# Optimization experiments

Hardware: AMD Instinct MI355X
Metric: run time of the kernel (lower is better)

Reference implementation:

```python
import jax, jax.numpy as jnp
import numpy as np

N, E, F_IN = 100000, 600000, 128
HID, NCLS = 128, 2
# ratio=0.8 applied three times: ceil(0.8*100000), ceil(0.8*80000), ceil(0.8*64000)
K1, K2, K3 = 80000, 64000, 51200


def setup_inputs() -> dict:
    key = jax.random.key(0)
    k = jax.random.split(key, 16)
    s = 0.05
    p = {}
    p['x'] = jax.random.normal(k[0], (N, F_IN), dtype=jnp.float32)
    p['edge_index'] = jax.random.randint(k[1], (2, E), 0, N)
    # GraphConv i: out = lin_rel(sum_j x_j) + lin_root(x_i); lin_root has no bias (PyG)
    p['Wr1'] = jax.random.normal(k[2], (HID, F_IN), jnp.float32) * s
    p['br1'] = jnp.zeros((HID,), jnp.float32)
    p['Wroot1'] = jax.random.normal(k[3], (HID, F_IN), jnp.float32) * s
    p['pw1'] = jax.random.normal(k[4], (HID,), jnp.float32) * s
    p['Wr2'] = jax.random.normal(k[5], (HID, HID), jnp.float32) * s
    p['br2'] = jnp.zeros((HID,), jnp.float32)
    p['Wroot2'] = jax.random.normal(k[6], (HID, HID), jnp.float32) * s
    p['pw2'] = jax.random.normal(k[7], (HID,), jnp.float32) * s
    p['Wr3'] = jax.random.normal(k[8], (HID, HID), jnp.float32) * s
    p['br3'] = jnp.zeros((HID,), jnp.float32)
    p['Wroot3'] = jax.random.normal(k[9], (HID, HID), jnp.float32) * s
    p['pw3'] = jax.random.normal(k[10], (HID,), jnp.float32) * s
    p['W_lin1'] = jax.random.normal(k[11], (HID, 2 * HID), jnp.float32) * s
    p['b_lin1'] = jnp.zeros((HID,), jnp.float32)
    p['W_lin2'] = jax.random.normal(k[12], (64, HID), jnp.float32) * s
    p['b_lin2'] = jnp.zeros((64,), jnp.float32)
    p['W_lin3'] = jax.random.normal(k[13], (NCLS, 64), jnp.float32) * s
    p['b_lin3'] = jnp.zeros((NCLS,), jnp.float32)
    return p


def _gconv(x, src, dst, emask, Wr, br, Wroot):
    # PyG GraphConv(aggr='add'): masked edges contribute zero (== removed edge)
    msg = x[src] * emask[:, None].astype(x.dtype)           # [E, F]
    agg = jax.ops.segment_sum(msg, dst, num_segments=x.shape[0])
    return agg @ Wr.T + br + x @ Wroot.T


def _topk_pool(x, src, dst, emask, w, k):
    # PyG TopKPooling: score = tanh((x.w)/||w||); keep top-k nodes; x = x[perm]*score[perm]
    score = jnp.tanh((x @ w) / jnp.linalg.norm(w))
    vals, perm = jax.lax.top_k(score, k)
    x_new = x[perm] * vals[:, None]
    new_idx = jnp.full((x.shape[0],), -1, jnp.int32).at[perm].set(
        jnp.arange(k, dtype=jnp.int32))
    ns, nd = new_idx[src], new_idx[dst]
    valid = emask & (ns >= 0) & (nd >= 0)
    return x_new, jnp.where(valid, ns, 0), jnp.where(valid, nd, 0), valid


def _readout(x):
    # single graph (batch=None): gmp || gap -> [1, 2F]
    return jnp.concatenate([x.max(axis=0), x.mean(axis=0)])[None, :]


def reference(x, edge_index, Wr1, br1, Wroot1, pw1, Wr2, br2, Wroot2, pw2,
              Wr3, br3, Wroot3, pw3, W_lin1, b_lin1, W_lin2, b_lin2, W_lin3, b_lin3):
    src = edge_index[0].astype(jnp.int32)
    dst = edge_index[1].astype(jnp.int32)
    emask = jnp.ones((src.shape[0],), dtype=bool)

    h = jax.nn.relu(_gconv(x, src, dst, emask, Wr1, br1, Wroot1))
    h, src, dst, emask = _topk_pool(h, src, dst, emask, pw1, K1)
    r1 = _readout(h)

    h = jax.nn.relu(_gconv(h, src, dst, emask, Wr2, br2, Wroot2))
    h, src, dst, emask = _topk_pool(h, src, dst, emask, pw2, K2)
    r2 = _readout(h)

    h = jax.nn.relu(_gconv(h, src, dst, emask, Wr3, br3, Wroot3))
    h, src, dst, emask = _topk_pool(h, src, dst, emask, pw3, K3)
    r3 = _readout(h)

    z = r1 + r2 + r3                                        # [1, 256]
    z = jax.nn.relu(z @ W_lin1.T + b_lin1)                  # dropout: inference no-op
    z = jax.nn.relu(z @ W_lin2.T + b_lin2)
    return z @ W_lin3.T + b_lin3                            # [1, num_classes]
```

## Files before the change

### kernel.cpp

```cpp
#include <hip/hip_runtime.h>
#include <hip/hip_bf16.h>
#include <math.h>

#define N0 100000
#define E0 600000
#define KP1 80000
#define KP2 64000
#define KP3 51200
#define F 128
#define SCAN_CHUNK 1024
#define NCHUNK ((N0 + SCAN_CHUNK - 1) / SCAN_CHUNK)
#define MAXGB 6400

typedef __attribute__((ext_vector_type(8))) short short8;
typedef __attribute__((ext_vector_type(8))) unsigned short ushort8;
typedef __attribute__((ext_vector_type(4))) float f32x4;

__device__ __forceinline__ unsigned fkey(float f) {
    unsigned u = __float_as_uint(f);
    return u ^ ((u & 0x80000000u) ? 0xFFFFFFFFu : 0x80000000u);
}
__device__ __forceinline__ unsigned short f2b(float f) {
    __hip_bfloat16 h = __float2bfloat16(f);
    return *(unsigned short*)&h;
}
__device__ __forceinline__ float b2f(unsigned short u) {
    __hip_bfloat16 h;
    *(unsigned short*)&h = u;
    return __bfloat162float(h);
}

__global__ __launch_bounds__(256) void cvt4K(const float* __restrict__ in,
                                             unsigned short* __restrict__ out, int n4,
                                             unsigned* __restrict__ bar, unsigned* __restrict__ hist,
                                             unsigned* __restrict__ cnt, int* __restrict__ orig) {
    int i = blockIdx.x * 256 + threadIdx.x;
    if (blockIdx.x == 0) {
        if (threadIdx.x < 16) bar[threadIdx.x] = 0u;
        hist[threadIdx.x] = 0u;
    }
    if (i < N0) { cnt[i] = 0u; orig[i] = i; }
    if (i >= n4) return;
    float4 v = *(const float4*)(in + (size_t)i * 4);
    *(ushort4*)(out + (size_t)i * 4) = make_ushort4(f2b(v.x), f2b(v.y), f2b(v.z), f2b(v.w));
}

__global__ __launch_bounds__(256) void cvtWAllK(const float* __restrict__ a0, const float* __restrict__ a1,
                                                const float* __restrict__ a2, const float* __restrict__ a3,
                                                const float* __restrict__ a4, const float* __restrict__ a5,
                                                unsigned short* __restrict__ o) {
    int m = blockIdx.y;
    const float* src = (m == 0) ? a0 : (m == 1) ? a1 : (m == 2) ? a2 : (m == 3) ? a3 : (m == 4) ? a4 : a5;
    int i = blockIdx.x * 256 + threadIdx.x;
    float4 v = *(const float4*)(src + (size_t)i * 4);
    *(ushort4*)(o + (size_t)m * 16384 + (size_t)i * 4) = make_ushort4(f2b(v.x), f2b(v.y), f2b(v.z), f2b(v.w));
}

__global__ __launch_bounds__(128) void pwnK(const float* __restrict__ p0, const float* __restrict__ p1,
                                            const float* __restrict__ p2, float* __restrict__ pwn) {
    __shared__ float sh[128];
    int l = blockIdx.x, t = threadIdx.x;
    const float* p = (l == 0) ? p0 : (l == 1) ? p1 : p2;
    float v = p[t];
    sh[t] = v * v;
    __syncthreads();
    for (int off = 64; off; off >>= 1) {
        if (t < off) sh[t] += sh[t + off];
        __syncthreads();
    }
    pwn[l * 128 + t] = v / sqrtf(sh[0]);
}

__global__ __launch_bounds__(256) void histDstK(const int* __restrict__ dst, unsigned* __restrict__ cnt) {
    int e = blockIdx.x * 256 + threadIdx.x;
    if (e < E0) atomicAdd(&cnt[dst[e]], 1u);
}

__global__ __launch_bounds__(256) void scanReduceK(const unsigned* __restrict__ cnt,
                                                   unsigned* __restrict__ chunkSum, int nbins) {
    __shared__ unsigned sh[256];
    int base = blockIdx.x * SCAN_CHUNK + threadIdx.x * 4;
    unsigned s = 0;
#pragma unroll
    for (int i = 0; i < 4; i++) { int b = base + i; if (b < nbins) s += cnt[b]; }
    sh[threadIdx.x] = s;
    __syncthreads();
    for (int off = 128; off; off >>= 1) {
        if (threadIdx.x < off) sh[threadIdx.x] += sh[threadIdx.x + off];
        __syncthreads();
    }
    if (threadIdx.x == 0) chunkSum[blockIdx.x] = sh[0];
}

__global__ void scanChunksK(const unsigned* __restrict__ chunkSum, unsigned* __restrict__ chunkOff,
                            int nchunks, unsigned* __restrict__ totalOut) {
    if (threadIdx.x == 0) {
        unsigned run = 0;
        for (int i = 0; i < nchunks; i++) { chunkOff[i] = run; run += chunkSum[i]; }
        *totalOut = run;
    }
}

__global__ __launch_bounds__(256) void scanFinalK(const unsigned* __restrict__ cntIn,
                                                  unsigned* __restrict__ cnt,
                                                  const unsigned* __restrict__ chunkOff,
                                                  unsigned* __restrict__ rowptr, int nbins) {
    __shared__ unsigned sh[256];
    int t = threadIdx.x;
    int base = blockIdx.x * SCAN_CHUNK + t * 4;
    unsigned c[4], s = 0;
#pragma unroll
    for (int i = 0; i < 4; i++) { int b = base + i; c[i] = (b < nbins) ? cntIn[b] : 0u; s += c[i]; }
    sh[t] = s;
    __syncthreads();
    for (int off = 1; off < 256; off <<= 1) {
        unsigned v = (t >= off) ? sh[t - off] : 0u;
        __syncthreads();
        sh[t] += v;
        __syncthreads();
    }
    unsigned basep = chunkOff[blockIdx.x] + sh[t] - s;
#pragma unroll
    for (int i = 0; i < 4; i++) {
        int b = base + i;
        if (b < nbins) { rowptr[b] = basep; basep += c[i]; cnt[b] = 0u; }
    }
}

__global__ __launch_bounds__(256) void scatterFillK(const int* __restrict__ src,
                                                    const int* __restrict__ dst,
                                                    const unsigned* __restrict__ rowptr,
                                                    unsigned* __restrict__ fill,
                                                    int* __restrict__ sortedSrc) {
    int e = blockIdx.x * 256 + threadIdx.x;
    if (e >= E0) return;
    int d = dst[e];
    unsigned p = rowptr[d] + atomicAdd(&fill[d], 1u);
    sortedSrc[p] = src[e];
}

__global__ __launch_bounds__(256) void aggSegB(const unsigned short* __restrict__ x,
                                               const int* __restrict__ srcCur,
                                               const unsigned* __restrict__ rowptr,
                                               const int* __restrict__ orig,
                                               unsigned short* __restrict__ agg, int n) {
    int g = blockIdx.x * 16 + (threadIdx.x >> 4);
    int q = threadIdx.x & 15;
    if (g >= n) return;
    int d = orig[g];
    unsigned e0 = rowptr[d], e1 = rowptr[d + 1];
    float a[8];
#pragma unroll
    for (int j = 0; j < 8; j++) a[j] = 0.f;
    unsigned e = e0;
    for (; e + 4 <= e1; e += 4) {
        int s0 = srcCur[e], s1 = srcCur[e + 1], s2 = srcCur[e + 2], s3 = srcCur[e + 3];
        ushort8 v0 = *(const ushort8*)(x + (size_t)(s0 < 0 ? 0 : s0) * F + q * 8);
        ushort8 v1 = *(const ushort8*)(x + (size_t)(s1 < 0 ? 0 : s1) * F + q * 8);
        ushort8 v2 = *(const ushort8*)(x + (size_t)(s2 < 0 ? 0 : s2) * F + q * 8);
        ushort8 v3 = *(const ushort8*)(x + (size_t)(s3 < 0 ? 0 : s3) * F + q * 8);
        float m0 = s0 < 0 ? 0.f : 1.f, m1 = s1 < 0 ? 0.f : 1.f;
        float m2 = s2 < 0 ? 0.f : 1.f, m3 = s3 < 0 ? 0.f : 1.f;
#pragma unroll
        for (int j = 0; j < 8; j++) {
            a[j] = fmaf(b2f(v0[j]), m0, a[j]);
            a[j] = fmaf(b2f(v1[j]), m1, a[j]);
            a[j] = fmaf(b2f(v2[j]), m2, a[j]);
            a[j] = fmaf(b2f(v3[j]), m3, a[j]);
        }
    }
    for (; e < e1; e++) {
        int s = srcCur[e];
        if (s < 0) continue;
        ushort8 v = *(const ushort8*)(x + (size_t)s * F + q * 8);
#pragma unroll
        for (int j = 0; j < 8; j++) a[j] += b2f(v[j]);
    }
    ushort8 o;
#pragma unroll
    for (int j = 0; j < 8; j++) o[j] = f2b(a[j]);
    *(ushort8*)(agg + (size_t)g * F + q * 8) = o;
}

#define CPAD 40
__global__ __launch_bounds__(256) void convM(const unsigned short* __restrict__ A0,
                                             const unsigned short* __restrict__ A1,
                                             const unsigned short* __restrict__ W0,
                                             const unsigned short* __restrict__ W1,
                                             const float* __restrict__ br,
                                             const float* __restrict__ pwn,
                                             unsigned short* __restrict__ hbf,
                                             float* __restrict__ sc,
                                             unsigned* __restrict__ keys,
                                             unsigned* __restrict__ hist,
                                             unsigned* __restrict__ st,
                                             unsigned* __restrict__ done,
                                             int n, int k, int nbGrid) {
    __shared__ unsigned short As[128 * CPAD];
    __shared__ unsigned short Bs[128 * CPAD];
    __shared__ unsigned selh[256];
    int tid = threadIdx.x;
    int w = tid >> 6, l = tid & 63;
    int r = l & 15, g = l >> 4;
    int bm = blockIdx.x * 128;
    int srow = tid >> 2, q4 = tid & 3;

    selh[tid] = 0u;

    f32x4 acc[2][8];
#pragma unroll
    for (int m = 0; m < 2; m++)
#pragma unroll
        for (int c = 0; c < 8; c++) acc[m][c] = (f32x4){0.f, 0.f, 0.f, 0.f};

    for (int ph = 0; ph < 2; ph++) {
        const unsigned short* A = ph ? A1 : A0;
        const unsigned short* W = ph ? W1 : W0;
        for (int kk = 0; kk < 128; kk += 32) {
            __syncthreads();
#pragma unroll
            for (int h2 = 0; h2 < 2; h2++) {
                int rr = srow + h2 * 64;
                uint4 av = make_uint4(0u, 0u, 0u, 0u);
                if (bm + rr < n) av = *(const uint4*)(A + (size_t)(bm + rr) * F + kk + q4 * 8);
                *(uint4*)(&As[rr * CPAD + q4 * 8]) = av;
                uint4 wv = *(const uint4*)(W + (size_t)rr * F + kk + q4 * 8);
                *(uint4*)(&Bs[rr * CPAD + q4 * 8]) = wv;
            }
            __syncthreads();
            short8 af[2], bf[8];
#pragma unroll
            for (int m = 0; m < 2; m++)
                af[m] = *(const short8*)(&As[(w * 32 + m * 16 + r) * CPAD + g * 8]);
#pragma unroll
            for (int c = 0; c < 8; c++)
                bf[c] = *(const short8*)(&Bs[(c * 16 + r) * CPAD + g * 8]);
#pragma unroll
            for (int m = 0; m < 2; m++)
#pragma unroll
                for (int c = 0; c < 8; c++)
                    acc[m][c] = __builtin_amdgcn_mfma_f32_16x16x32_bf16(af[m], bf[c], acc[m][c], 0, 0, 0);
        }
    }

    float pd[2][4];
#pragma unroll
    for (int m = 0; m < 2; m++)
#pragma unroll
        for (int j = 0; j < 4; j++) pd[m][j] = 0.f;

#pragma unroll
    for (int c = 0; c < 8; c++) {
        int col = c * 16 + r;
        float bias = br[col];
        float pwc = pwn[col];
#pragma unroll
        for (int m = 0; m < 2; m++) {
#pragma unroll
            for (int j = 0; j < 4; j++) {
                int row = bm + w * 32 + m * 16 + g * 4 + j;
                float h = fmaxf(acc[m][c][j] + bias, 0.f);
                pd[m][j] += h * pwc;
                if (row < n) hbf[(size_t)row * F + col] = f2b(h);
            }
        }
    }
#pragma unroll
    for (int m = 0; m < 2; m++) {
#pragma unroll
        for (int j = 0; j < 4; j++) {
            float p = pd[m][j];
            p += __shfl_xor(p, 1);
            p += __shfl_xor(p, 2);
            p += __shfl_xor(p, 4);
            p += __shfl_xor(p, 8);
            if (r == 0) {
                int row = bm + w * 32 + m * 16 + g * 4 + j;
                if (row < n) {
                    float s = tanhf(p);
                    sc[row] = s;
                    unsigned key = fkey(s);
                    keys[row] = key;
                    atomicAdd(&selh[key >> 24], 1u);
                }
            }
        }
    }

    __syncthreads();
    if (selh[tid]) atomicAdd(&hist[tid], selh[tid]);
    __syncthreads();
    __shared__ bool lastS;
    if (tid == 0) {
        __threadfence();
        lastS = (atomicAdd(done, 1u) == (unsigned)(nbGrid - 1));
    }
    __syncthreads();
    if (!lastS) return;
    selh[tid] = atomicExch(&hist[tid], 0u);
    __syncthreads();
    if (tid == 0) {
        unsigned krem = (unsigned)k, cum = 0, pfx = 0;
        for (int bch = 255; bch >= 0; bch--) {
            unsigned cc = selh[bch];
            if (cum + cc >= krem) {
                pfx = ((unsigned)bch) << 24;
                krem -= cum;
                break;
            }
            cum += cc;
        }
        atomicExch(&st[0], pfx);
        atomicExch(&st[1], krem);
        *done = 0u;
    }
}

__global__ __launch_bounds__(256) void histSelK(const unsigned* __restrict__ keys, int n,
                                                int p, unsigned* __restrict__ st,
                                                unsigned* __restrict__ hist,
                                                unsigned* __restrict__ done, int nb) {
    __shared__ unsigned lh[256];
    __shared__ bool last;
    int tid = threadIdx.x;
    lh[tid] = 0;
    __syncthreads();
    unsigned prefix = st[0];
    int i = blockIdx.x * 256 + tid;
    if (i < n) {
        unsigned key = keys[i];
        bool m = ((key >> (32 - 8 * p)) == (prefix >> (32 - 8 * p)));
        if (m) atomicAdd(&lh[(key >> (24 - 8 * p)) & 255u], 1u);
    }
    __syncthreads();
    if (lh[tid]) atomicAdd(&hist[tid], lh[tid]);
    __syncthreads();
    if (tid == 0) {
        __threadfence();
        last = (atomicAdd(done, 1u) == (unsigned)(nb - 1));
    }
    __syncthreads();
    if (!last) return;
    lh[tid] = atomicExch(&hist[tid], 0u);
    __syncthreads();
    if (tid == 0) {
        unsigned krem = st[1], cum = 0;
        for (int b = 255; b >= 0; b--) {
            unsigned c = lh[b];
            if (cum + c >= krem) {
                st[0] |= ((unsigned)b) << (24 - 8 * p);
                st[1] = krem - cum;
                break;
            }
            cum += c;
        }
        *done = 0u;
    }
}

__global__ __launch_bounds__(256) void countsK(const unsigned* __restrict__ keys, int n,
                                               const unsigned* __restrict__ st,
                                               unsigned* __restrict__ bGT, unsigned* __restrict__ bEQ,
                                               unsigned* __restrict__ sGT, unsigned* __restrict__ sEQ,
                                               unsigned* __restrict__ done, int nb) {
    __shared__ int cg_, ce_;
    __shared__ bool last;
    __shared__ unsigned sgl[128], seq[128];
    int tid = threadIdx.x;
    if (tid == 0) { cg_ = 0; ce_ = 0; }
    __syncthreads();
    unsigned t = st[0];
    int g = 0, e = 0;
    for (int it = 0; it < 4; it++) {
        int i = blockIdx.x * 1024 + it * 256 + tid;
        if (i < n) {
            unsigned k = keys[i];
            g += (k > t);
            e += (k == t);
        }
    }
    atomicAdd(&cg_, g);
    atomicAdd(&ce_, e);
    __syncthreads();
    if (tid == 0) {
        bGT[blockIdx.x] = (unsigned)cg_;
        bEQ[blockIdx.x] = (unsigned)ce_;
        __threadfence();
        last = (atomicAdd(done, 1u) == (unsigned)(nb - 1));
    }
    __syncthreads();
    if (!last) return;
    if (tid < nb && tid < 128) { sgl[tid] = atomicAdd(&bGT[tid], 0u); seq[tid] = atomicAdd(&bEQ[tid], 0u); }
    __syncthreads();
    if (tid == 0) {
        unsigned gs = 0, es = 0;
        for (int b = 0; b < nb; b++) {
            atomicExch(&sGT[b], gs);
            atomicExch(&sEQ[b], es);
            gs += sgl[b];
            es += seq[b];
        }
        *done = 0u;
    }
}

__global__ __launch_bounds__(256) void markOrigK(const unsigned* __restrict__ keys, int n,
                                                 const unsigned* __restrict__ st,
                                                 const unsigned* __restrict__ sGT,
                                                 const unsigned* __restrict__ sEQ,
                                                 int* __restrict__ nidx,
                                                 const int* __restrict__ origIn,
                                                 int* __restrict__ origOut, int doNext) {
    __shared__ int wG[4], wE[4];
    __shared__ int runG, runE;
    int tid = threadIdx.x, wv = tid >> 6, lane = tid & 63;
    if (tid == 0) { runG = 0; runE = 0; }
    unsigned t = st[0];
    int needEq = (int)st[1];
    int gOff = (int)atomicAdd((unsigned*)&sGT[blockIdx.x], 0u);
    int eOff = (int)atomicAdd((unsigned*)&sEQ[blockIdx.x], 0u);
    unsigned long long mlt = (((unsigned long long)1) << lane) - 1ull;
    __syncthreads();
    for (int it = 0; it < 4; it++) {
        int i = blockIdx.x * 1024 + it * 256 + tid;
        bool inb = i < n;
        unsigned k = inb ? keys[i] : 0u;
        bool pG = inb && (k > t), pE = inb && (k == t);
        unsigned long long bG = __ballot(pG), bE = __ballot(pE);
        int lpG = __popcll(bG & mlt), lpE = __popcll(bE & mlt);
        if (lane == 0) { wG[wv] = __popcll(bG); wE[wv] = __popcll(bE); }
        __syncthreads();
        int woG = 0, woE = 0;
        for (int w = 0; w < wv; w++) { woG += wG[w]; woE += wE[w]; }
        int gB = gOff + runG + woG + lpG;
        int eB = eOff + runE + woE + lpE;
        int ni = -1;
        if (pG) ni = gB + (eB < needEq ? eB : needEq);
        else if (pE && eB < needEq) ni = gB + eB;
        if (inb) {
            nidx[i] = ni;
            if (doNext && ni >= 0) origOut[ni] = origIn[i];
        }
        __syncthreads();
        if (tid == 0) {
            runG += wG[0] + wG[1] + wG[2] + wG[3];
            runE += wE[0] + wE[1] + wE[2] + wE[3];
        }
        __syncthreads();
    }
}

__global__ __launch_bounds__(256) void gatherRK(const unsigned short* __restrict__ hbf,
                                                const float* __restrict__ sc,
                                                const int* __restrict__ nidx,
                                                const int* __restrict__ srcIn,
                                                int* __restrict__ srcOut,
                                                unsigned short* __restrict__ bufB,
                                                float* __restrict__ pmax, float* __restrict__ psum,
                                                int n, int doNext) {
    __shared__ float redm[256 * 8];
    __shared__ float reds[256 * 8];
    int tid = threadIdx.x, b = blockIdx.x;
    int q = tid & 15;
    int i = b * 16 + (tid >> 4);
    float lm[8], ls[8];
#pragma unroll
    for (int j = 0; j < 8; j++) { lm[j] = -INFINITY; ls[j] = 0.f; }
    if (i < n) {
        int ni = nidx[i];
        if (ni >= 0) {
            float s = sc[i];
            ushort8 v = *(const ushort8*)(hbf + (size_t)i * F + q * 8);
            ushort8 o;
#pragma unroll
            for (int j = 0; j < 8; j++) {
                float prod = b2f(v[j]) * s;
                o[j] = f2b(prod);
                lm[j] = fmaxf(lm[j], prod);
                ls[j] += prod;
            }
            *(ushort8*)(bufB + (size_t)ni * F + q * 8) = o;
        }
    }
    if (doNext) {
        int nbg = gridDim.x;
        for (int e = b * 256 + tid; e < E0; e += nbg * 256) {
            int s2 = srcIn[e];
            srcOut[e] = (s2 >= 0) ? nidx[s2] : -1;
        }
    }
#pragma unroll
    for (int j = 0; j < 8; j++) { redm[tid * 8 + j] = lm[j]; reds[tid * 8 + j] = ls[j]; }
    __syncthreads();
    if (tid < 16) {
        for (int g2 = 1; g2 < 16; g2++) {
#pragma unroll
            for (int j = 0; j < 8; j++) {
                lm[j] = fmaxf(lm[j], redm[(g2 * 16 + tid) * 8 + j]);
                ls[j] += reds[(g2 * 16 + tid) * 8 + j];
            }
        }
#pragma unroll
        for (int j = 0; j < 8; j++) {
            pmax[(size_t)b * 128 + tid * 8 + j] = lm[j];
            psum[(size_t)b * 128 + tid * 8 + j] = ls[j];
        }
    }
}

__global__ __launch_bounds__(128) void rfinal2K(const float* __restrict__ pmax,
                                                const float* __restrict__ psum,
                                                unsigned* __restrict__ pm2, unsigned* __restrict__ ps2,
                                                float* __restrict__ r, unsigned* __restrict__ done,
                                                int np, int k, int initR) {
    int t = threadIdx.x, b = blockIdx.x;
    float m = -INFINITY, s = 0.f;
    for (int row = b; row < np; row += 64) {
        m = fmaxf(m, pmax[(size_t)row * 128 + t]);
        s += psum[(size_t)row * 128 + t];
    }
    atomicExch(&pm2[b * 128 + t], __float_as_uint(m));
    atomicExch(&ps2[b * 128 + t], __float_as_uint(s));
    __syncthreads();
    __shared__ bool last;
    if (t == 0) {
        __threadfence();
        last = (atomicAdd(done, 1u) == 63u);
    }
    __syncthreads();
    if (!last) return;
    m = -INFINITY; s = 0.f;
#pragma unroll 8
    for (int bb = 0; bb < 64; bb++) {
        m = fmaxf(m, __uint_as_float(atomicAdd(&pm2[bb * 128 + t], 0u)));
        s += __uint_as_float(atomicAdd(&ps2[bb * 128 + t], 0u));
    }
    if (initR) { r[t] = m; r[128 + t] = s / (float)k; }
    else       { r[t] += m; r[128 + t] += s / (float)k; }
    if (t == 0) *done = 0u;
}

__global__ __launch_bounds__(256) void mlpK(const float* __restrict__ r,
                                            const float* __restrict__ W1, const float* __restrict__ b1,
                                            const float* __restrict__ W2, const float* __restrict__ b2,
                                            const float* __restrict__ W3, const float* __restrict__ b3,
                                            float* __restrict__ out) {
    __shared__ float z0[256], z1[128], z2[64];
    int t = threadIdx.x;
    z0[t] = r[t];
    __syncthreads();
    if (t < 128) {
        float a = b1[t];
        for (int kk = 0; kk < 256; kk++) a = fmaf(W1[t * 256 + kk], z0[kk], a);
        z1[t] = fmaxf(a, 0.f);
    }
    __syncthreads();
    if (t < 64) {
        float a = b2[t];
        for (int kk = 0; kk < 128; kk++) a = fmaf(W2[t * 128 + kk], z1[kk], a);
        z2[t] = fmaxf(a, 0.f);
    }
    __syncthreads();
    if (t < 2) {
        float a = b3[t];
        for (int kk = 0; kk < 64; kk++) a = fmaf(W3[t * 64 + kk], z2[kk], a);
        out[t] = a;
    }
}

extern "C" void kernel_launch(void* const* d_in, const int* in_sizes, int n_in,
                              void* d_out, int out_size, void* d_ws, size_t ws_size,
                              hipStream_t stream) {
    const float* x = (const float*)d_in[0];
    const int* ei = (const int*)d_in[1];
    const float* Wr[3]    = { (const float*)d_in[2],  (const float*)d_in[6],  (const float*)d_in[10] };
    const float* br[3]    = { (const float*)d_in[3],  (const float*)d_in[7],  (const float*)d_in[11] };
    const float* Wroot[3] = { (const float*)d_in[4],  (const float*)d_in[8],  (const float*)d_in[12] };
    const float* pw[3]    = { (const float*)d_in[5],  (const float*)d_in[9],  (const float*)d_in[13] };
    const float* W1 = (const float*)d_in[14];
    const float* b1 = (const float*)d_in[15];
    const float* W2 = (const float*)d_in[16];
    const float* b2 = (const float*)d_in[17];
    const float* W3 = (const float*)d_in[18];
    const float* b3 = (const float*)d_in[19];
    float* out = (float*)d_out;
    char* w = (char*)d_ws;

    size_t o = 0;
    auto alc = [&](size_t bytes) { size_t r = o; o += (bytes + 255) & ~(size_t)255; return r; };
    unsigned short* hbf    = (unsigned short*)(w + alc((size_t)N0 * F * 2));
    unsigned short* xbf    = (unsigned short*)(w + alc((size_t)N0 * F * 2));
    unsigned short* aggbf  = (unsigned short*)(w + alc((size_t)N0 * F * 2));
    unsigned short* bufBbf = (unsigned short*)(w + alc((size_t)KP1 * F * 2));
    unsigned short* wbf    = (unsigned short*)(w + alc((size_t)6 * 16384 * 2));
    float*    pwn    = (float*)(w + alc(3 * 128 * 4));
    float*    sc     = (float*)(w + alc((size_t)N0 * 4));
    unsigned* keys   = (unsigned*)(w + alc((size_t)N0 * 4));
    int*      nidx   = (int*)(w + alc((size_t)N0 * 4));
    int*      sSrc0  = (int*)(w + alc((size_t)E0 * 4));
    int*      srcCA  = (int*)(w + alc((size_t)E0 * 4));
    int*      srcCB  = (int*)(w + alc((size_t)E0 * 4));
    unsigned* cnt    = (unsigned*)(w + alc((size_t)N0 * 4));
    unsigned* rowptr = (unsigned*)(w + alc((size_t)(N0 + 1) * 4));
    int*      origA  = (int*)(w + alc((size_t)N0 * 4));
    int*      origB  = (int*)(w + alc((size_t)N0 * 4));
    unsigned* chS    = (unsigned*)(w + alc(NCHUNK * 4));
    unsigned* chO    = (unsigned*)(w + alc(NCHUNK * 4));
    unsigned* hist   = (unsigned*)(w + alc(256 * 4));
    unsigned* st     = (unsigned*)(w + alc(64));
    unsigned* barA   = (unsigned*)(w + alc(16 * 4));
    unsigned* bGT    = (unsigned*)(w + alc(128 * 4));
    unsigned* bEQ    = (unsigned*)(w + alc(128 * 4));
    unsigned* sGT    = (unsigned*)(w + alc(128 * 4));
    unsigned* sEQ    = (unsigned*)(w + alc(128 * 4));
    float*    r      = (float*)(w + alc(256 * 4));
    float*    pmax   = (float*)(w + alc((size_t)MAXGB * F * 4));
    float*    psum   = (float*)(w + alc((size_t)MAXGB * F * 4));
    unsigned* pm2    = (unsigned*)(w + alc(64 * 128 * 4));
    unsigned* ps2    = (unsigned*)(w + alc(64 * 128 * 4));
    if (o > ws_size) return;

    const int* srcOrig = ei;
    const int* dstOrig = ei + E0;

    cvt4K<<<(N0 * F / 4 + 255) / 256, 256, 0, stream>>>(x, xbf, N0 * F / 4, barA, hist, cnt, origA);
    cvtWAllK<<<dim3(16, 6), 256, 0, stream>>>(Wr[0], Wroot[0], Wr[1], Wroot[1], Wr[2], Wroot[2], wbf);
    pwnK<<<3, 128, 0, stream>>>(pw[0], pw[1], pw[2], pwn);
    histDstK<<<(E0 + 255) / 256, 256, 0, stream>>>(dstOrig, cnt);
    scanReduceK<<<NCHUNK, 256, 0, stream>>>(cnt, chS, N0);
    scanChunksK<<<1, 1, 0, stream>>>(chS, chO, NCHUNK, rowptr + N0);
    scanFinalK<<<NCHUNK, 256, 0, stream>>>(cnt, cnt, chO, rowptr, N0);
    scatterFillK<<<(E0 + 255) / 256, 256, 0, stream>>>(srcOrig, dstOrig, rowptr, cnt, sSrc0);

    unsigned* doneA = barA + 8;

    const int ns[3] = { N0, KP1, KP2 };
    const int ks[3] = { KP1, KP2, KP3 };
    const int* srcCur[3] = { sSrc0, srcCA, srcCB };
    int* srcNext[3] = { srcCA, srcCB, srcCA };
    const int* origCur[3] = { origA, origB, origA };
    int* origNext[3] = { origB, origA, origB };

    for (int L = 0; L < 3; L++) {
        int n = ns[L], k = ks[L];
        const unsigned short* xinbf = (L == 0) ? xbf : bufBbf;
        int doNext = (L < 2) ? 1 : 0;

        aggSegB<<<(n + 15) / 16, 256, 0, stream>>>(xinbf, srcCur[L], rowptr, origCur[L], aggbf, n);
        int nbc = (n + 127) / 128;
        convM<<<nbc, 256, 0, stream>>>(aggbf, xinbf,
                                       wbf + (size_t)(L * 2) * 16384,
                                       wbf + (size_t)(L * 2 + 1) * 16384,
                                       br[L], pwn + L * 128, hbf, sc, keys,
                                       hist, st, doneA, n, k, nbc);
        int nbh = (n + 255) / 256;
        for (int p = 1; p < 4; p++)
            histSelK<<<nbh, 256, 0, stream>>>(keys, n, p, st, hist, doneA, nbh);
        int nb = (n + 1023) / 1024;
        countsK<<<nb, 256, 0, stream>>>(keys, n, st, bGT, bEQ, sGT, sEQ, doneA, nb);
        markOrigK<<<nb, 256, 0, stream>>>(keys, n, st, sGT, sEQ, nidx, origCur[L], origNext[L], doNext);
        int nbg = (n + 15) / 16;
        gatherRK<<<nbg, 256, 0, stream>>>(hbf, sc, nidx, srcCur[L], srcNext[L], bufBbf, pmax, psum, n, doNext);
        rfinal2K<<<64, 128, 0, stream>>>(pmax, psum, pm2, ps2, r, doneA, nbg, k, (L == 0) ? 1 : 0);
    }

    mlpK<<<1, 256, 0, stream>>>(r, W1, b1, W2, b2, W3, b3, out);
}
```

Before: 618.3 us.

## Fuse setup and selection kernels using grid-wide spin barriers

Merges the input and weight conversion and pw normalisation into one setup kernel. Folds the chunk scan into the reduce kernel via a last-block pattern. Replaces the three radix-select histogram launches with one kernel that uses grid-wide atomic spin barriers, and merges counting with compaction the same way. The goal is to cut kernel launch overhead and gaps, but the grid barriers assume all blocks (up to 391) are co-resident, which risks deadlock and adds spin cost.

```diff
diff --git a/kernel.cpp b/kernel.cpp
--- a/kernel.cpp
+++ b/kernel.cpp
@@ -11,6 +11,9 @@
 #define SCAN_CHUNK 1024
 #define NCHUNK ((N0 + SCAN_CHUNK - 1) / SCAN_CHUNK)
 #define MAXGB 6400
+#define NBCVT 12500
+#define NBW 96
+#define NBHD ((E0 + 255) / 256)
 
 typedef __attribute__((ext_vector_type(8))) short short8;
 typedef __attribute__((ext_vector_type(8))) unsigned short ushort8;
@@ -30,45 +33,62 @@
     return __bfloat162float(h);
 }
 
-__global__ __launch_bounds__(256) void cvt4K(const float* __restrict__ in,
-                                             unsigned short* __restrict__ out, int n4,
-                                             unsigned* __restrict__ bar, unsigned* __restrict__ hist,
-                                             unsigned* __restrict__ cnt, int* __restrict__ orig) {
-    int i = blockIdx.x * 256 + threadIdx.x;
-    if (blockIdx.x == 0) {
-        if (threadIdx.x < 16) bar[threadIdx.x] = 0u;
-        hist[threadIdx.x] = 0u;
-    }
-    if (i < N0) { cnt[i] = 0u; orig[i] = i; }
-    if (i >= n4) return;
-    float4 v = *(const float4*)(in + (size_t)i * 4);
-    *(ushort4*)(out + (size_t)i * 4) = make_ushort4(f2b(v.x), f2b(v.y), f2b(v.z), f2b(v.w));
-}
-
-__global__ __launch_bounds__(256) void cvtWAllK(const float* __restrict__ a0, const float* __restrict__ a1,
-                                                const float* __restrict__ a2, const float* __restrict__ a3,
-                                                const float* __restrict__ a4, const float* __restrict__ a5,
-                                                unsigned short* __restrict__ o) {
-    int m = blockIdx.y;
-    const float* src = (m == 0) ? a0 : (m == 1) ? a1 : (m == 2) ? a2 : (m == 3) ? a3 : (m == 4) ? a4 : a5;
-    int i = blockIdx.x * 256 + threadIdx.x;
-    float4 v = *(const float4*)(src + (size_t)i * 4);
-    *(ushort4*)(o + (size_t)m * 16384 + (size_t)i * 4) = make_ushort4(f2b(v.x), f2b(v.y), f2b(v.z), f2b(v.w));
-}
-
-__global__ __launch_bounds__(128) void pwnK(const float* __restrict__ p0, const float* __restrict__ p1,
-                                            const float* __restrict__ p2, float* __restrict__ pwn) {
-    __shared__ float sh[128];
-    int l = blockIdx.x, t = threadIdx.x;
-    const float* p = (l == 0) ? p0 : (l == 1) ? p1 : p2;
-    float v = p[t];
-    sh[t] = v * v;
-    __syncthreads();
-    for (int off = 64; off; off >>= 1) {
-        if (t < off) sh[t] += sh[t + off];
-        __syncthreads();
-    }
-    pwn[l * 128 + t] = v / sqrtf(sh[0]);
+__device__ __forceinline__ void gbarT(unsigned* bar, unsigned target) {
+    __threadfence();
+    __syncthreads();
+    if (threadIdx.x == 0) {
+        atomicAdd(bar, 1u);
+        while (atomicAdd(bar, 0u) < target) __builtin_amdgcn_s_sleep(1);
+        __threadfence();
+    }
+    __syncthreads();
+}
+
+__global__ __launch_bounds__(256) void setupK(const float* __restrict__ x, unsigned short* __restrict__ xbf,
+                                              const float* __restrict__ a0, const float* __restrict__ a1,
+                                              const float* __restrict__ a2, const float* __restrict__ a3,
+                                              const float* __restrict__ a4, const float* __restrict__ a5,
+                                              unsigned short* __restrict__ wbf,
+                                              const float* __restrict__ p0, const float* __restrict__ p1,
+                                              const float* __restrict__ p2, float* __restrict__ pwn,
+                                              unsigned* __restrict__ cnt, int* __restrict__ orig,
+                                              unsigned* __restrict__ bar, unsigned* __restrict__ hist) {
+    __shared__ float shf[128];
+    int b = blockIdx.x, tid = threadIdx.x;
+    if (b < NBCVT) {
+        if (b == 0) {
+            if (tid < 16) bar[tid] = 0u;
+            for (int j = tid; j < 2560; j += 256) hist[j] = 0u;
+        }
+        int i = b * 256 + tid;
+        if (i < N0) { cnt[i] = 0u; orig[i] = i; }
+        if (i < N0 * F / 4) {
+            float4 v = *(const float4*)(x + (size_t)i * 4);
+            *(ushort4*)(xbf + (size_t)i * 4) = make_ushort4(f2b(v.x), f2b(v.y), f2b(v.z), f2b(v.w));
+        }
+    } else if (b < NBCVT + NBW) {
+        int bb = b - NBCVT;
+        int m = bb >> 4;
+        const float* src = (m == 0) ? a0 : (m == 1) ? a1 : (m == 2) ? a2 : (m == 3) ? a3 : (m == 4) ? a4 : a5;
+        int i = (bb & 15) * 256 + tid;
+        float4 v = *(const float4*)(src + (size_t)i * 4);
+        *(ushort4*)(wbf + (size_t)m * 16384 + (size_t)i * 4) = make_ushort4(f2b(v.x), f2b(v.y), f2b(v.z), f2b(v.w));
+    } else {
+        for (int l = 0; l < 3; l++) {
+            const float* p = (l == 0) ? p0 : (l == 1) ? p1 : p2;
+            float v = 0.f;
+            if (tid < 128) { v = p[tid]; shf[tid] = v * v; }
+            __syncthreads();
+            for (int off = 64; off; off >>= 1) {
+                if (tid < off) shf[tid] += shf[tid + off];
+                __syncthreads();
+            }
+            float nrm = sqrtf(shf[0]);
+            __syncthreads();
+            if (tid < 128) pwn[l * 128 + tid] = v / nrm;
+            __syncthreads();
+        }
+    }
 }
 
 __global__ __launch_bounds__(256) void histDstK(const int* __restrict__ dst, unsigned* __restrict__ cnt) {
@@ -76,28 +96,39 @@
     if (e < E0) atomicAdd(&cnt[dst[e]], 1u);
 }
 
-__global__ __launch_bounds__(256) void scanReduceK(const unsigned* __restrict__ cnt,
-                                                   unsigned* __restrict__ chunkSum, int nbins) {
+__global__ __launch_bounds__(256) void scanRedFusedK(const unsigned* __restrict__ cnt,
+                                                     unsigned* __restrict__ chunkSum,
+                                                     unsigned* __restrict__ chunkOff,
+                                                     unsigned* __restrict__ rowptr,
+                                                     unsigned* __restrict__ done, int nbins) {
     __shared__ unsigned sh[256];
-    int base = blockIdx.x * SCAN_CHUNK + threadIdx.x * 4;
+    __shared__ bool last;
+    int tid = threadIdx.x;
+    int base = blockIdx.x * SCAN_CHUNK + tid * 4;
     unsigned s = 0;
 #pragma unroll
     for (int i = 0; i < 4; i++) { int b = base + i; if (b < nbins) s += cnt[b]; }
-    sh[threadIdx.x] = s;
+    sh[tid] = s;
     __syncthreads();
     for (int off = 128; off; off >>= 1) {
-        if (threadIdx.x < off) sh[threadIdx.x] += sh[threadIdx.x + off];
-        __syncthreads();
-    }
-    if (threadIdx.x == 0) chunkSum[blockIdx.x] = sh[0];
-}
-
-__global__ void scanChunksK(const unsigned* __restrict__ chunkSum, unsigned* __restrict__ chunkOff,
-                            int nchunks, unsigned* __restrict__ totalOut) {
-    if (threadIdx.x == 0) {
+        if (tid < off) sh[tid] += sh[tid + off];
+        __syncthreads();
+    }
+    if (tid == 0) {
+        atomicExch(&chunkSum[blockIdx.x], sh[0]);
+        __threadfence();
+        last = (atomicAdd(done, 1u) == (unsigned)(NCHUNK - 1));
+    }
+    __syncthreads();
+    if (!last) return;
+    if (tid == 0) {
         unsigned run = 0;
-        for (int i = 0; i < nchunks; i++) { chunkOff[i] = run; run += chunkSum[i]; }
-        *totalOut = run;
+        for (int i = 0; i < NCHUNK; i++) {
+            atomicExch(&chunkOff[i], run);
+            run += atomicAdd(&chunkSum[i], 0u);
+        }
+        rowptr[N0] = run;
+        *done = 0u;
     }
 }
 
@@ -119,7 +150,7 @@
         sh[t] += v;
         __syncthreads();
     }
-    unsigned basep = chunkOff[blockIdx.x] + sh[t] - s;
+    unsigned basep = atomicAdd((unsigned*)&chunkOff[blockIdx.x], 0u) + sh[t] - s;
 #pragma unroll
     for (int i = 0; i < 4; i++) {
         int b = base + i;
@@ -316,113 +347,100 @@
     }
 }
 
-__global__ __launch_bounds__(256) void histSelK(const unsigned* __restrict__ keys, int n,
-                                                int p, unsigned* __restrict__ st,
-                                                unsigned* __restrict__ hist,
-                                                unsigned* __restrict__ done, int nb) {
+__global__ __launch_bounds__(256) void sel3K(const unsigned* __restrict__ keys, int n,
+                                             unsigned* __restrict__ st,
+                                             unsigned* __restrict__ ghist,
+                                             unsigned* __restrict__ bar, int nb) {
     __shared__ unsigned lh[256];
-    __shared__ bool last;
-    int tid = threadIdx.x;
-    lh[tid] = 0;
-    __syncthreads();
-    unsigned prefix = st[0];
-    int i = blockIdx.x * 256 + tid;
-    if (i < n) {
-        unsigned key = keys[i];
-        bool m = ((key >> (32 - 8 * p)) == (prefix >> (32 - 8 * p)));
-        if (m) atomicAdd(&lh[(key >> (24 - 8 * p)) & 255u], 1u);
-    }
-    __syncthreads();
-    if (lh[tid]) atomicAdd(&hist[tid], lh[tid]);
-    __syncthreads();
-    if (tid == 0) {
-        __threadfence();
-        last = (atomicAdd(done, 1u) == (unsigned)(nb - 1));
-    }
-    __syncthreads();
-    if (!last) return;
-    lh[tid] = atomicExch(&hist[tid], 0u);
-    __syncthreads();
-    if (tid == 0) {
-        unsigned krem = st[1], cum = 0;
-        for (int b = 255; b >= 0; b--) {
-            unsigned c = lh[b];
-            if (cum + c >= krem) {
-                st[0] |= ((unsigned)b) << (24 - 8 * p);
-                st[1] = krem - cum;
-                break;
-            }
-            cum += c;
-        }
-        *done = 0u;
-    }
-}
-
-__global__ __launch_bounds__(256) void countsK(const unsigned* __restrict__ keys, int n,
-                                               const unsigned* __restrict__ st,
-                                               unsigned* __restrict__ bGT, unsigned* __restrict__ bEQ,
-                                               unsigned* __restrict__ sGT, unsigned* __restrict__ sEQ,
-                                               unsigned* __restrict__ done, int nb) {
+    __shared__ unsigned sPfx, sKrem;
+    int tid = threadIdx.x, b = blockIdx.x;
+    if (tid == 0) { sPfx = st[0]; sKrem = st[1]; }
+    __syncthreads();
+    unsigned pfx = sPfx, krem = sKrem;
+    int i = b * 256 + tid;
+    for (int p = 1; p <= 3; p++) {
+        int sh = 32 - 8 * p;
+        lh[tid] = 0;
+        __syncthreads();
+        if (i < n) {
+            unsigned key = keys[i];
+            if ((key >> sh) == (pfx >> sh))
+                atomicAdd(&lh[(key >> (sh - 8)) & 255u], 1u);
+        }
+        __syncthreads();
+        unsigned* gh = ghist + (p - 1) * 256;
+        if (lh[tid]) atomicAdd(&gh[tid], lh[tid]);
+        gbarT(bar, (unsigned)(p * nb));
+        lh[tid] = atomicAdd(&gh[tid], 0u);
+        __syncthreads();
+        if (tid == 0) {
+            unsigned cum = 0;
+            for (int bch = 255; bch >= 0; bch--) {
+                unsigned cc = lh[bch];
+                if (cum + cc >= krem) {
+                    sPfx = pfx | (((unsigned)bch) << (sh - 8));
+                    sKrem = krem - cum;
+                    break;
+                }
+                cum += cc;
+            }
+        }
+        __syncthreads();
+        pfx = sPfx;
+        krem = sKrem;
+    }
+    if (b == 0 && tid == 0) { atomicExch(&st[0], pfx); atomicExch(&st[1], krem); }
+}
+
+__global__ __launch_bounds__(256) void countMarkK(const unsigned* __restrict__ keys, int n,
+                                                  const unsigned* __restrict__ st,
+                                                  unsigned* __restrict__ bGT, unsigned* __restrict__ bEQ,
+                                                  int* __restrict__ nidx,
+                                                  const int* __restrict__ origIn,
+                                                  int* __restrict__ origOut, int doNext,
+                                                  unsigned* __restrict__ bar, int nb) {
     __shared__ int cg_, ce_;
-    __shared__ bool last;
     __shared__ unsigned sgl[128], seq[128];
-    int tid = threadIdx.x;
-    if (tid == 0) { cg_ = 0; ce_ = 0; }
-    __syncthreads();
-    unsigned t = st[0];
-    int g = 0, e = 0;
-    for (int it = 0; it < 4; it++) {
-        int i = blockIdx.x * 1024 + it * 256 + tid;
-        if (i < n) {
-            unsigned k = keys[i];
-            g += (k > t);
-            e += (k == t);
-        }
-    }
-    atomicAdd(&cg_, g);
-    atomicAdd(&ce_, e);
-    __syncthreads();
-    if (tid == 0) {
-        bGT[blockIdx.x] = (unsigned)cg_;
-        bEQ[blockIdx.x] = (unsigned)ce_;
-        __threadfence();
-        last = (atomicAdd(done, 1u) == (unsigned)(nb - 1));
-    }
-    __syncthreads();
-    if (!last) return;
-    if (tid < nb && tid < 128) { sgl[tid] = atomicAdd(&bGT[tid], 0u); seq[tid] = atomicAdd(&bEQ[tid], 0u); }
-    __syncthreads();
-    if (tid == 0) {
-        unsigned gs = 0, es = 0;
-        for (int b = 0; b < nb; b++) {
-            atomicExch(&sGT[b], gs);
-            atomicExch(&sEQ[b], es);
-            gs += sgl[b];
-            es += seq[b];
-        }
-        *done = 0u;
-    }
-}
-
-__global__ __launch_bounds__(256) void markOrigK(const unsigned* __restrict__ keys, int n,
-                                                 const unsigned* __restrict__ st,
-                                                 const unsigned* __restrict__ sGT,
-                                                 const unsigned* __restrict__ sEQ,
-                                                 int* __restrict__ nidx,
-                                                 const int* __restrict__ origIn,
-                                                 int* __restrict__ origOut, int doNext) {
     __shared__ int wG[4], wE[4];
-    __shared__ int runG, runE;
-    int tid = threadIdx.x, wv = tid >> 6, lane = tid & 63;
-    if (tid == 0) { runG = 0; runE = 0; }
+    __shared__ int runG, runE, shGOff, shEOff;
+    int tid = threadIdx.x, b = blockIdx.x;
+    int wv = tid >> 6, lane = tid & 63;
+    if (tid == 0) { cg_ = 0; ce_ = 0; runG = 0; runE = 0; }
+    __syncthreads();
     unsigned t = st[0];
     int needEq = (int)st[1];
-    int gOff = (int)atomicAdd((unsigned*)&sGT[blockIdx.x], 0u);
-    int eOff = (int)atomicAdd((unsigned*)&sEQ[blockIdx.x], 0u);
+    {
+        int g = 0, e = 0;
+#pragma unroll
+        for (int it = 0; it < 4; it++) {
+            int i = b * 1024 + it * 256 + tid;
+            if (i < n) {
+                unsigned k = keys[i];
+                g += (k > t);
+                e += (k == t);
+            }
+        }
+        atomicAdd(&cg_, g);
+        atomicAdd(&ce_, e);
+    }
+    __syncthreads();
+    if (tid == 0) {
+        atomicExch(&bGT[b], (unsigned)cg_);
+        atomicExch(&bEQ[b], (unsigned)ce_);
+    }
+    gbarT(bar, (unsigned)nb);
+    if (tid < nb) { sgl[tid] = atomicAdd(&bGT[tid], 0u); seq[tid] = atomicAdd(&bEQ[tid], 0u); }
+    __syncthreads();
+    if (tid == 0) {
+        int gs = 0, es = 0;
+        for (int bb = 0; bb < b; bb++) { gs += (int)sgl[bb]; es += (int)seq[bb]; }
+        shGOff = gs; shEOff = es;
+    }
+    __syncthreads();
+    int gOff = shGOff, eOff = shEOff;
     unsigned long long mlt = (((unsigned long long)1) << lane) - 1ull;
-    __syncthreads();
     for (int it = 0; it < 4; it++) {
-        int i = blockIdx.x * 1024 + it * 256 + tid;
+        int i = b * 1024 + it * 256 + tid;
         bool inb = i < n;
         unsigned k = inb ? keys[i] : 0u;
         bool pG = inb && (k > t), pE = inb && (k == t);
@@ -431,7 +449,7 @@
         if (lane == 0) { wG[wv] = __popcll(bG); wE[wv] = __popcll(bE); }
         __syncthreads();
         int woG = 0, woE = 0;
-        for (int w = 0; w < wv; w++) { woG += wG[w]; woE += wE[w]; }
+        for (int w2 = 0; w2 < wv; w2++) { woG += wG[w2]; woE += wE[w2]; }
         int gB = gOff + runG + woG + lpG;
         int eB = eOff + runE + woE + lpE;
         int ni = -1;
@@ -606,13 +624,11 @@
     int*      origB  = (int*)(w + alc((size_t)N0 * 4));
     unsigned* chS    = (unsigned*)(w + alc(NCHUNK * 4));
     unsigned* chO    = (unsigned*)(w + alc(NCHUNK * 4));
-    unsigned* hist   = (unsigned*)(w + alc(256 * 4));
+    unsigned* hist   = (unsigned*)(w + alc(2560 * 4));
     unsigned* st     = (unsigned*)(w + alc(64));
     unsigned* barA   = (unsigned*)(w + alc(16 * 4));
     unsigned* bGT    = (unsigned*)(w + alc(128 * 4));
     unsigned* bEQ    = (unsigned*)(w + alc(128 * 4));
-    unsigned* sGT    = (unsigned*)(w + alc(128 * 4));
-    unsigned* sEQ    = (unsigned*)(w + alc(128 * 4));
     float*    r      = (float*)(w + alc(256 * 4));
     float*    pmax   = (float*)(w + alc((size_t)MAXGB * F * 4));
     float*    psum   = (float*)(w + alc((size_t)MAXGB * F * 4));
@@ -623,16 +639,14 @@
     const int* srcOrig = ei;
     const int* dstOrig = ei + E0;
 
-    cvt4K<<<(N0 * F / 4 + 255) / 256, 256, 0, stream>>>(x, xbf, N0 * F / 4, barA, hist, cnt, origA);
-    cvtWAllK<<<dim3(16, 6), 256, 0, stream>>>(Wr[0], Wroot[0], Wr[1], Wroot[1], Wr[2], Wroot[2], wbf);
-    pwnK<<<3, 128, 0, stream>>>(pw[0], pw[1], pw[2], pwn);
-    histDstK<<<(E0 + 255) / 256, 256, 0, stream>>>(dstOrig, cnt);
-    scanReduceK<<<NCHUNK, 256, 0, stream>>>(cnt, chS, N0);
-    scanChunksK<<<1, 1, 0, stream>>>(chS, chO, NCHUNK, rowptr + N0);
+    setupK<<<NBCVT + NBW + 1, 256, 0, stream>>>(x, xbf,
+                                                Wr[0], Wroot[0], Wr[1], Wroot[1], Wr[2], Wroot[2], wbf,
+                                                pw[0], pw[1], pw[2], pwn, cnt, origA, barA, hist);
+    unsigned* doneA = barA + 8;
+    histDstK<<<NBHD, 256, 0, stream>>>(dstOrig, cnt);
+    scanRedFusedK<<<NCHUNK, 256, 0, stream>>>(cnt, chS, chO, rowptr, doneA, N0);
     scanFinalK<<<NCHUNK, 256, 0, stream>>>(cnt, cnt, chO, rowptr, N0);
-    scatterFillK<<<(E0 + 255) / 256, 256, 0, stream>>>(srcOrig, dstOrig, rowptr, cnt, sSrc0);
-
-    unsigned* doneA = barA + 8;
+    scatterFillK<<<NBHD, 256, 0, stream>>>(srcOrig, dstOrig, rowptr, cnt, sSrc0);
 
     const int ns[3] = { N0, KP1, KP2 };
     const int ks[3] = { KP1, KP2, KP3 };
@@ -654,11 +668,10 @@
                                        br[L], pwn + L * 128, hbf, sc, keys,
                                        hist, st, doneA, n, k, nbc);
         int nbh = (n + 255) / 256;
-        for (int p = 1; p < 4; p++)
-            histSelK<<<nbh, 256, 0, stream>>>(keys, n, p, st, hist, doneA, nbh);
+        sel3K<<<nbh, 256, 0, stream>>>(keys, n, st, hist + 256 + L * 768, barA + 1 + L, nbh);
         int nb = (n + 1023) / 1024;
-        countsK<<<nb, 256, 0, stream>>>(keys, n, st, bGT, bEQ, sGT, sEQ, doneA, nb);
-        markOrigK<<<nb, 256, 0, stream>>>(keys, n, st, sGT, sEQ, nidx, origCur[L], origNext[L], doNext);
+        countMarkK<<<nb, 256, 0, stream>>>(keys, n, st, bGT, bEQ, nidx,
+                                           origCur[L], origNext[L], doNext, barA + 4 + L, nb);
         int nbg = (n + 15) / 16;
         gatherRK<<<nbg, 256, 0, stream>>>(hbf, sc, nidx, srcCur[L], srcNext[L], bufBbf, pmax, psum, n, doNext);
         rfinal2K<<<64, 128, 0, stream>>>(pmax, psum, pm2, ps2, r, doneA, nbg, k, (L == 0) ? 1 : 0);
```

After: 907.6 us. 46.8% more time.
